# Kernel optimization log

Measured on AMD Instinct MI355X. Metric: run time of the kernel, lower is better.

The kernel has to match this reference:

```python
import jax, jax.numpy as jnp
import numpy as np


def conv1x1(x, w, b):
    # x: [B,C,H,W], w: [O,C], b: [O]
    return jnp.einsum('oc,bchw->bohw', w, x) + b[None, :, None, None]


def interp_bilinear_ac(x, oh, ow):
    # bilinear resize with align_corners=True, x: [B,C,H,W] -> [B,C,oh,ow]
    B, C, H, W = x.shape
    if (H, W) == (oh, ow):
        return x
    ys = jnp.linspace(0.0, H - 1.0, oh)
    xs = jnp.linspace(0.0, W - 1.0, ow)
    y0 = jnp.clip(jnp.floor(ys).astype(jnp.int32), 0, H - 1)
    y1 = jnp.minimum(y0 + 1, H - 1)
    x0 = jnp.clip(jnp.floor(xs).astype(jnp.int32), 0, W - 1)
    x1 = jnp.minimum(x0 + 1, W - 1)
    wy = (ys - y0).astype(x.dtype)
    wx = (xs - x0).astype(x.dtype)
    top = x[:, :, y0, :] * (1 - wy)[None, None, :, None] + x[:, :, y1, :] * wy[None, None, :, None]
    out = top[:, :, :, x0] * (1 - wx)[None, None, None, :] + top[:, :, :, x1] * wx[None, None, None, :]
    return out


def non_local(x, qw, qb, kw, kb, vw, vb, ow_, ob):
    B, C, H, W = x.shape
    HW = H * W
    q = conv1x1(x, qw, qb).reshape(B, -1, HW)  # [B, Ci, HW]
    k = conv1x1(x, kw, kb).reshape(B, -1, HW)
    v = conv1x1(x, vw, vb).reshape(B, -1, HW)
    attn = jnp.einsum('bci,bcj->bij', q, k)     # [B, HW, HW]
    attn = jax.nn.softmax(attn, axis=-1)
    out = jnp.einsum('bcj,bij->bci', v, attn)   # [B, Ci, HW]
    out = out.reshape(B, -1, H, W)
    return conv1x1(out, ow_, ob)


def _forward(x1, x2, x3, x4, qw, qb, kw, kb, vw, vb, ow_, ob, g1w, g1b, g2w, g2b):
    H1, W1 = x1.shape[2], x1.shape[3]
    x2_up = interp_bilinear_ac(x2, H1, W1)
    x3_up = interp_bilinear_ac(x3, H1, W1)
    x4_up = interp_bilinear_ac(x4, H1, W1)
    gf = jnp.concatenate([x1, x2_up, x3_up, x4_up], axis=1)  # [B, 128, H1, W1]
    gf = non_local(gf, qw, qb, kw, kb, vw, vb, ow_, ob)
    h = jax.nn.relu(conv1x1(gf, g1w, g1b))
    sw = jax.nn.sigmoid(conv1x1(h, g2w, g2b))                # [B, 128, H1, W1]
    w1, w2, w3, w4 = sw[:, :32], sw[:, 32:64], sw[:, 64:96], sw[:, 96:128]
    x1_out = x1 * (1 + w1)
    x2_out = x2 * (1 + interp_bilinear_ac(w2, x2.shape[2], x2.shape[3]))
    x3_out = x3 * (1 + interp_bilinear_ac(w3, x3.shape[2], x3.shape[3]))
    x4_out = x4 * (1 + interp_bilinear_ac(w4, x4.shape[2], x4.shape[3]))
    return (x1_out, x2_out, x3_out, x4_out)


def setup_inputs() -> dict:
    key = jax.random.key(0)
    ks = jax.random.split(key, 16)
    C = 128  # channel*4
    Ci = 64  # inter_channel
    Cg = 32
    d = {
        'x1': jax.random.normal(ks[0], (8, 32, 64, 64), jnp.float32),
        'x2': jax.random.normal(ks[1], (8, 32, 32, 32), jnp.float32),
        'x3': jax.random.normal(ks[2], (8, 32, 16, 16), jnp.float32),
        'x4': jax.random.normal(ks[3], (8, 32, 8, 8), jnp.float32),
        'qw': jax.random.normal(ks[4], (Ci, C), jnp.float32) * 0.05,
        'qb': jnp.zeros((Ci,), jnp.float32),
        'kw': jax.random.normal(ks[5], (Ci, C), jnp.float32) * 0.05,
        'kb': jnp.zeros((Ci,), jnp.float32),
        'vw': jax.random.normal(ks[6], (Ci, C), jnp.float32) * 0.05,
        'vb': jnp.zeros((Ci,), jnp.float32),
        'ow_': jax.random.normal(ks[7], (C, Ci), jnp.float32) * 0.05,
        'ob': jnp.zeros((C,), jnp.float32),
        'g1w': jax.random.normal(ks[8], (Cg, C), jnp.float32) * 0.05,
        'g1b': jnp.zeros((Cg,), jnp.float32),
        'g2w': jax.random.normal(ks[9], (C, Cg), jnp.float32) * 0.05,
        'g2b': jnp.zeros((C,), jnp.float32),
    }
    return d


def reference(x1, x2, x3, x4, qw, qb, kw, kb, vw, vb, ow_, ob, g1w, g1b, g2w, g2b):
    return _forward(x1, x2, x3, x4, qw, qb, kw, kb, vw, vb, ow_, ob, g1w, g1b, g2w, g2b)
```

## Files before the change

kernel.cpp:

```cpp
#include <hip/hip_runtime.h>
#include <hip/hip_bf16.h>


typedef __attribute__((ext_vector_type(8))) short s16x8;
typedef __attribute__((ext_vector_type(4))) float f32x4;

#define LOG2E 1.44269504088896340736f

__device__ __forceinline__ unsigned int f2bf(float f) {
    unsigned int u = __float_as_uint(f);
    u += 0x7fffu + ((u >> 16) & 1u);
    return u >> 16;
}
__device__ __forceinline__ unsigned int pk2bf(float a, float b) {
    union { __hip_bfloat162 h; unsigned int u; } cv;
    cv.h = __float22bfloat162_rn(make_float2(a, b));
    return cv.u;
}
__device__ __forceinline__ float bf2f(unsigned short u) {
    return __uint_as_float((unsigned int)u << 16);
}
__device__ __forceinline__ float fexp2(float x) { return __builtin_amdgcn_exp2f(x); }
__device__ __forceinline__ float frcp(float x)  { return __builtin_amdgcn_rcpf(x); }
__device__ __forceinline__ s16x8 cvt8(const float* __restrict__ p, float scale) {
    float4 a = ((const float4*)p)[0];
    float4 b = ((const float4*)p)[1];
    union { s16x8 v; uint4 u; } cv;
    cv.u.x = pk2bf(a.x * scale, a.y * scale);
    cv.u.y = pk2bf(a.z * scale, a.w * scale);
    cv.u.z = pk2bf(b.x * scale, b.y * scale);
    cv.u.w = pk2bf(b.z * scale, b.w * scale);
    return cv.v;
}

__global__ __launch_bounds__(256, 4) void k_qkv(
    const float* __restrict__ x1, const float* __restrict__ x2,
    const float* __restrict__ x3, const float* __restrict__ x4,
    const float* __restrict__ qw, const float* __restrict__ qb,
    const float* __restrict__ kw, const float* __restrict__ kb,
    const float* __restrict__ vw, const float* __restrict__ vb,
    unsigned short* __restrict__ Qg, unsigned short* __restrict__ Kg,
    unsigned short* __restrict__ Vg) {
  __shared__ __align__(16) unsigned short gfb[32 * 136];
  unsigned int* gfbu = (unsigned int*)gfb;

  const int blk = blockIdx.x;
  const int b = blk >> 7;
  const int i0 = (blk & 127) << 5;
  const int t = threadIdx.x;
  const int wv = t >> 6, lane = t & 63;
  const int r = lane & 15, qd = lane >> 4;
  f32x4 zf = {0.f, 0.f, 0.f, 0.f};

  {
    const int cp = t >> 2, q = t & 3;
    const int c0 = cp << 1;
    const int pbase = q << 3;
    const int oy = i0 >> 6;
    const int ox0 = (i0 & 63) | (q << 3);

    if (cp < 16) {
      const float* s0 = x1 + (((b * 32 + c0) << 12) + (oy << 6) + ox0);
      const float* s1 = s0 + 4096;
      #pragma unroll
      for (int k4 = 0; k4 < 2; k4++) {
        float4 va = ((const float4*)s0)[k4];
        float4 vb = ((const float4*)s1)[k4];
        int p = pbase + k4 * 4;
        gfbu[(p + 0) * 68 + cp] = pk2bf(va.x, vb.x);
        gfbu[(p + 1) * 68 + cp] = pk2bf(va.y, vb.y);
        gfbu[(p + 2) * 68 + cp] = pk2bf(va.z, vb.z);
        gfbu[(p + 3) * 68 + cp] = pk2bf(va.w, vb.w);
      }
    } else {
      const float* base; int S, cs;
      if (cp < 32)      { base = x2; S = 32; cs = c0 - 32; }
      else if (cp < 48) { base = x3; S = 16; cs = c0 - 64; }
      else              { base = x4; S = 8;  cs = c0 - 96; }
      const float* pl0 = base + (b * 32 + cs) * S * S;
      const float* pl1 = pl0 + S * S;
      float yf = (float)oy * (float)(S - 1) * (1.0f / 63.0f);
      int y0 = (int)yf; if (y0 > S - 1) y0 = S - 1;
      int y1 = y0 + 1;  if (y1 > S - 1) y1 = S - 1;
      float wy = yf - (float)y0;
      const float* r00 = pl0 + y0 * S; const float* r01 = pl0 + y1 * S;
      const float* r10 = pl1 + y0 * S; const float* r11 = pl1 + y1 * S;
      for (int k = 0; k < 8; k++) {
        int ox = ox0 + k;
        float xf = (float)ox * (float)(S - 1) * (1.0f / 63.0f);
        int xx0 = (int)xf; if (xx0 > S - 1) xx0 = S - 1;
        int xx1 = xx0 + 1; if (xx1 > S - 1) xx1 = S - 1;
        float wx = xf - (float)xx0;
        float a0 = r00[xx0] + wx * (r00[xx1] - r00[xx0]);
        float b0 = r01[xx0] + wx * (r01[xx1] - r01[xx0]);
        float v0 = a0 + wy * (b0 - a0);
        float a1 = r10[xx0] + wx * (r10[xx1] - r10[xx0]);
        float b1 = r11[xx0] + wx * (r11[xx1] - r11[xx0]);
        float v1 = a1 + wy * (b1 - a1);
        gfbu[(pbase + k) * 68 + cp] = pk2bf(v0, v1);
      }
    }
  }
  __syncthreads();

  const int ocb = wv * 48;
  s16x8 af[3][4];
  float4 bias[3];
  #pragma unroll
  for (int mti = 0; mti < 3; mti++) {
    const int goc = ocb + mti * 16;
    const float* wsrc; const float* bsrc; float scale;
    if (goc < 64)       { wsrc = qw + goc * 128;         bsrc = qb + goc;         scale = LOG2E; }
    else if (goc < 128) { wsrc = kw + (goc - 64) * 128;  bsrc = kb + (goc - 64);  scale = 1.0f; }
    else                { wsrc = vw + (goc - 128) * 128; bsrc = vb + (goc - 128); scale = 1.0f; }
    #pragma unroll
    for (int ks = 0; ks < 4; ks++)
      af[mti][ks] = cvt8(wsrc + r * 128 + ks * 32 + qd * 8, scale);
    float4 bv = *(const float4*)(bsrc + qd * 4);
    bias[mti] = make_float4(bv.x * scale, bv.y * scale, bv.z * scale, bv.w * scale);
  }

  #pragma unroll
  for (int nt = 0; nt < 2; nt++) {
    s16x8 bfr[4];
    #pragma unroll
    for (int ks = 0; ks < 4; ks++)
      bfr[ks] = *(const s16x8*)&gfb[(nt * 16 + r) * 136 + ks * 32 + qd * 8];
    f32x4 acc[3] = {zf, zf, zf};
    #pragma unroll
    for (int ks = 0; ks < 4; ks++)
      #pragma unroll
      for (int mti = 0; mti < 3; mti++)
        acc[mti] = __builtin_amdgcn_mfma_f32_16x16x32_bf16(af[mti][ks], bfr[ks], acc[mti], 0, 0, 0);

    const int pos = i0 + nt * 16 + r;
    #pragma unroll
    for (int mti = 0; mti < 3; mti++) {
      const int gmt = wv * 3 + mti;
      float ax = acc[mti].x + bias[mti].x;
      float ay = acc[mti].y + bias[mti].y;
      float az = acc[mti].z + bias[mti].z;
      float aw = acc[mti].w + bias[mti].w;
      if (gmt < 4) {
        uint2 w; w.x = pk2bf(ax, ay); w.y = pk2bf(az, aw);
        *(uint2*)&Qg[(((b << 12) + pos) << 6) + gmt * 16 + qd * 4] = w;
      } else if (gmt < 8) {
        uint2 w; w.x = pk2bf(ax, ay); w.y = pk2bf(az, aw);
        *(uint2*)&Kg[(((b << 12) + pos) << 6) + (gmt - 4) * 16 + qd * 4] = w;
      } else {
        int ocv = (gmt - 8) * 16 + qd * 4;
        Vg[((b * 64 + ocv + 0) << 12) + pos] = (unsigned short)f2bf(ax);
        Vg[((b * 64 + ocv + 1) << 12) + pos] = (unsigned short)f2bf(ay);
        Vg[((b * 64 + ocv + 2) << 12) + pos] = (unsigned short)f2bf(az);
        Vg[((b * 64 + ocv + 3) << 12) + pos] = (unsigned short)f2bf(aw);
      }
    }
  }
}

__global__ __launch_bounds__(256, 4) void k_attn(
    const unsigned short* __restrict__ Qg, const unsigned short* __restrict__ Kg,
    const unsigned short* __restrict__ Vg, unsigned short* __restrict__ Op,
    float* __restrict__ Lp) {
  __shared__ __align__(16) unsigned short Kl[64 * 72];
  __shared__ __align__(16) unsigned short Vl[64 * 72];
  __shared__ __align__(16) unsigned short Pl[4][32 * 72];

  const int b = blockIdx.x >> 7;
  const int part = (blockIdx.x >> 5) & 3;
  const int qg = blockIdx.x & 31;
  const int i0 = qg << 7;
  const int t = threadIdx.x;
  const int wv = t >> 6, lane = t & 63;
  const int r = lane & 15, qd = lane >> 4;
  const int qbase = i0 + wv * 32;

  s16x8 qf[2][2];
  #pragma unroll
  for (int nt = 0; nt < 2; nt++)
    #pragma unroll
    for (int ks = 0; ks < 2; ks++)
      qf[nt][ks] = *(const s16x8*)&Qg[(((b << 12) + qbase + nt * 16 + r) << 6) + ks * 32 + qd * 8];

  f32x4 zf = {0.f, 0.f, 0.f, 0.f};
  f32x4 acc[2][4];
  #pragma unroll
  for (int nt = 0; nt < 2; nt++)
    #pragma unroll
    for (int mt = 0; mt < 4; mt++) acc[nt][mt] = zf;
  f32x4 accl[2] = {zf, zf};

  const short ob = (r == 0) ? (short)0x3F80 : (short)0;
  const s16x8 vones = {ob, ob, ob, ob, ob, ob, ob, ob};

  const int srow = t >> 3, sseg = t & 7;
  const unsigned short* kt0 = &Kg[(((b << 12) + (part << 10) + srow) << 6) + sseg * 8];
  const unsigned short* vt0 = &Vg[((b * 64 + srow) << 12) + (part << 10) + sseg * 8];
  uint4 pk0 = *(const uint4*)(kt0);
  uint4 pk1 = *(const uint4*)(kt0 + (32 << 6));
  uint4 pv0 = *(const uint4*)(vt0);
  uint4 pv1 = *(const uint4*)(vt0 + (32 << 12));

  for (int it = 0; it < 16; it++) {
    __syncthreads();
    *(uint4*)&Kl[srow * 72 + sseg * 8] = pk0;
    *(uint4*)&Kl[(srow + 32) * 72 + sseg * 8] = pk1;
    *(uint4*)&Vl[srow * 72 + sseg * 8] = pv0;
    *(uint4*)&Vl[(srow + 32) * 72 + sseg * 8] = pv1;
    __syncthreads();
    if (it < 15) {
      int j0 = (it + 1) << 6;
      pk0 = *(const uint4*)(kt0 + (j0 << 6));
      pk1 = *(const uint4*)(kt0 + ((j0 + 32) << 6));
      pv0 = *(const uint4*)(vt0 + j0);
      pv1 = *(const uint4*)(vt0 + (32 << 12) + j0);
    }

    #pragma unroll
    for (int mt = 0; mt < 4; mt++) {
      s16x8 kf0 = *(const s16x8*)&Kl[(mt * 16 + r) * 72 + qd * 8];
      s16x8 kf1 = *(const s16x8*)&Kl[(mt * 16 + r) * 72 + 32 + qd * 8];
      #pragma unroll
      for (int nt = 0; nt < 2; nt++) {
        f32x4 s = __builtin_amdgcn_mfma_f32_16x16x32_bf16(kf0, qf[nt][0], zf, 0, 0, 0);
        s = __builtin_amdgcn_mfma_f32_16x16x32_bf16(kf1, qf[nt][1], s, 0, 0, 0);
        float px = fexp2(s.x);
        float py = fexp2(s.y);
        float pz = fexp2(s.z);
        float pw = fexp2(s.w);
        uint2 w;
        w.x = pk2bf(px, py);
        w.y = pk2bf(pz, pw);
        *(uint2*)&Pl[wv][(nt * 16 + r) * 72 + mt * 16 + qd * 4] = w;
      }
    }
    __builtin_amdgcn_wave_barrier();

    #pragma unroll
    for (int ks = 0; ks < 2; ks++) {
      s16x8 pf0 = *(const s16x8*)&Pl[wv][(r) * 72 + ks * 32 + qd * 8];
      s16x8 pf1 = *(const s16x8*)&Pl[wv][(16 + r) * 72 + ks * 32 + qd * 8];
      #pragma unroll
      for (int mt = 0; mt < 4; mt++) {
        s16x8 vf = *(const s16x8*)&Vl[(mt * 16 + r) * 72 + ks * 32 + qd * 8];
        acc[0][mt] = __builtin_amdgcn_mfma_f32_16x16x32_bf16(vf, pf0, acc[0][mt], 0, 0, 0);
        acc[1][mt] = __builtin_amdgcn_mfma_f32_16x16x32_bf16(vf, pf1, acc[1][mt], 0, 0, 0);
      }
      accl[0] = __builtin_amdgcn_mfma_f32_16x16x32_bf16(vones, pf0, accl[0], 0, 0, 0);
      accl[1] = __builtin_amdgcn_mfma_f32_16x16x32_bf16(vones, pf1, accl[1], 0, 0, 0);
    }
  }

  #pragma unroll
  for (int nt = 0; nt < 2; nt++) {
    float lv = __shfl(accl[nt].x, r);
    float inv = frcp(lv);
    int qrow = qbase + nt * 16 + r;
    unsigned short* orow = &Op[(((part * 8 + b) << 12) + qrow) << 6];
    #pragma unroll
    for (int mt = 0; mt < 4; mt++) {
      uint2 w;
      w.x = pk2bf(acc[nt][mt].x * inv, acc[nt][mt].y * inv);
      w.y = pk2bf(acc[nt][mt].z * inv, acc[nt][mt].w * inv);
      *(uint2*)&orow[mt * 16 + qd * 4] = w;
    }
    if (qd == 0) Lp[((part * 8 + b) << 12) + qrow] = lv;
  }
}

__global__ __launch_bounds__(256, 4) void k_out(
    const unsigned short* __restrict__ Op, const float* __restrict__ Lp,
    const float* __restrict__ ow, const float* __restrict__ obias,
    const float* __restrict__ g1w, const float* __restrict__ g1b,
    const float* __restrict__ g2w, const float* __restrict__ g2b,
    const float* __restrict__ x1, float* __restrict__ out,
    unsigned short* __restrict__ SWb) {
  __shared__ __align__(16) unsigned short Ot[32 * 72];
  __shared__ __align__(16) unsigned short gf2t[32 * 136];
  __shared__ __align__(16) unsigned short ht[32 * 40];
  const int blk = blockIdx.x;
  const int b = blk >> 7;
  const int i0 = (blk & 127) << 5;
  const int t = threadIdx.x;
  const int wv = t >> 6, lane = t & 63;
  const int r = lane & 15, qd = lane >> 4;
  f32x4 zf = {0.f, 0.f, 0.f, 0.f};

  {
    const int pos = t >> 3, seg = t & 7;
    const int i = i0 + pos;
    float lp4[4], lsum = 0.f;
    #pragma unroll
    for (int p = 0; p < 4; p++) { lp4[p] = Lp[((p * 8 + b) << 12) + i]; lsum += lp4[p]; }
    float o[8];
    #pragma unroll
    for (int k = 0; k < 8; k++) o[k] = 0.f;
    float invs = frcp(lsum);
    #pragma unroll
    for (int p = 0; p < 4; p++) {
      float w = lp4[p] * invs;
      uint4 u = *(const uint4*)&Op[((((p * 8 + b) << 12) + i) << 6) + seg * 8];
      o[0] += w * __uint_as_float(u.x << 16);
      o[1] += w * __uint_as_float(u.x & 0xFFFF0000u);
      o[2] += w * __uint_as_float(u.y << 16);
      o[3] += w * __uint_as_float(u.y & 0xFFFF0000u);
      o[4] += w * __uint_as_float(u.z << 16);
      o[5] += w * __uint_as_float(u.z & 0xFFFF0000u);
      o[6] += w * __uint_as_float(u.w << 16);
      o[7] += w * __uint_as_float(u.w & 0xFFFF0000u);
    }
    unsigned int* dst = (unsigned int*)&Ot[pos * 72 + seg * 8];
    #pragma unroll
    for (int k = 0; k < 4; k++) dst[k] = pk2bf(o[2 * k], o[2 * k + 1]);
  }
  __syncthreads();

  {
    const int ocb = wv * 32;
    s16x8 af[2][2];
    #pragma unroll
    for (int mt = 0; mt < 2; mt++)
      #pragma unroll
      for (int ks = 0; ks < 2; ks++)
        af[mt][ks] = cvt8(&ow[(ocb + mt * 16 + r) * 64 + ks * 32 + qd * 8], 1.0f);
    float4 bias[2];
    #pragma unroll
    for (int mt = 0; mt < 2; mt++)
      bias[mt] = *(const float4*)&obias[ocb + mt * 16 + qd * 4];
    #pragma unroll
    for (int nt = 0; nt < 2; nt++) {
      s16x8 bfr[2];
      #pragma unroll
      for (int ks = 0; ks < 2; ks++)
        bfr[ks] = *(const s16x8*)&Ot[(nt * 16 + r) * 72 + ks * 32 + qd * 8];
      f32x4 acc[2] = {zf, zf};
      #pragma unroll
      for (int ks = 0; ks < 2; ks++)
        #pragma unroll
        for (int mt = 0; mt < 2; mt++)
          acc[mt] = __builtin_amdgcn_mfma_f32_16x16x32_bf16(af[mt][ks], bfr[ks], acc[mt], 0, 0, 0);
      #pragma unroll
      for (int mt = 0; mt < 2; mt++) {
        uint2 w;
        w.x = pk2bf(acc[mt].x + bias[mt].x, acc[mt].y + bias[mt].y);
        w.y = pk2bf(acc[mt].z + bias[mt].z, acc[mt].w + bias[mt].w);
        *(uint2*)&gf2t[(nt * 16 + r) * 136 + ocb + mt * 16 + qd * 4] = w;
      }
    }
  }
  __syncthreads();

  {
    const int mt = wv & 1, pt = wv >> 1;
    s16x8 af[4];
    #pragma unroll
    for (int ks = 0; ks < 4; ks++)
      af[ks] = cvt8(&g1w[(mt * 16 + r) * 128 + ks * 32 + qd * 8], 1.0f);
    float4 bias = *(const float4*)&g1b[mt * 16 + qd * 4];
    s16x8 bfr[4];
    #pragma unroll
    for (int ks = 0; ks < 4; ks++)
      bfr[ks] = *(const s16x8*)&gf2t[(pt * 16 + r) * 136 + ks * 32 + qd * 8];
    f32x4 acc = zf;
    #pragma unroll
    for (int ks = 0; ks < 4; ks++)
      acc = __builtin_amdgcn_mfma_f32_16x16x32_bf16(af[ks], bfr[ks], acc, 0, 0, 0);
    uint2 w;
    w.x = pk2bf(fmaxf(acc.x + bias.x, 0.f), fmaxf(acc.y + bias.y, 0.f));
    w.y = pk2bf(fmaxf(acc.z + bias.z, 0.f), fmaxf(acc.w + bias.w, 0.f));
    *(uint2*)&ht[(pt * 16 + r) * 40 + mt * 16 + qd * 4] = w;
  }
  __syncthreads();

  {
    const int nb = wv * 32;
    s16x8 bfg[2];
    float bias[2];
    #pragma unroll
    for (int ntl = 0; ntl < 2; ntl++) {
      bfg[ntl] = cvt8(&g2w[(nb + ntl * 16 + r) * 32 + qd * 8], 1.0f);
      bias[ntl] = g2b[nb + ntl * 16 + r];
    }
    #pragma unroll
    for (int mt = 0; mt < 2; mt++) {
      s16x8 af = *(const s16x8*)&ht[(mt * 16 + r) * 40 + qd * 8];
      #pragma unroll
      for (int ntl = 0; ntl < 2; ntl++) {
        f32x4 acc = __builtin_amdgcn_mfma_f32_16x16x32_bf16(af, bfg[ntl], zf, 0, 0, 0);
        const int oc3 = nb + ntl * 16 + r;
        float s0 = frcp(1.0f + fexp2(-LOG2E * (acc.x + bias[ntl])));
        float s1 = frcp(1.0f + fexp2(-LOG2E * (acc.y + bias[ntl])));
        float s2 = frcp(1.0f + fexp2(-LOG2E * (acc.z + bias[ntl])));
        float s3 = frcp(1.0f + fexp2(-LOG2E * (acc.w + bias[ntl])));
        if (nb == 0) {
          const int off = ((b * 32 + oc3) << 12) + i0 + mt * 16 + qd * 4;
          float4 xv = *(const float4*)&x1[off];
          float4 o4;
          o4.x = xv.x * (1.f + s0); o4.y = xv.y * (1.f + s1);
          o4.z = xv.z * (1.f + s2); o4.w = xv.w * (1.f + s3);
          *(float4*)&out[off] = o4;
        } else {
          uint2 w; w.x = pk2bf(s0, s1); w.y = pk2bf(s2, s3);
          *(uint2*)&SWb[((b * 128 + oc3) << 12) + i0 + mt * 16 + qd * 4] = w;
        }
      }
    }
  }
}

__device__ __forceinline__ float bilin64(const unsigned short* __restrict__ p,
                                         int oy, int ox, int n) {
  float yf = (float)oy * 63.0f / (float)n;
  int y0 = (int)yf; if (y0 > 63) y0 = 63;
  int y1 = y0 + 1;  if (y1 > 63) y1 = 63;
  float wy = yf - (float)y0;
  float xf = (float)ox * 63.0f / (float)n;
  int x0 = (int)xf; if (x0 > 63) x0 = 63;
  int x1 = x0 + 1;  if (x1 > 63) x1 = 63;
  float wx = xf - (float)x0;
  float v00 = bf2f(p[y0 * 64 + x0]), v01 = bf2f(p[y0 * 64 + x1]);
  float v10 = bf2f(p[y1 * 64 + x0]), v11 = bf2f(p[y1 * 64 + x1]);
  float top = v00 + wx * (v01 - v00);
  float bot = v10 + wx * (v11 - v10);
  return top + wy * (bot - top);
}

__global__ __launch_bounds__(256) void k_final(
    const float* __restrict__ x2, const float* __restrict__ x3,
    const float* __restrict__ x4,
    const unsigned short* __restrict__ SWb, float* __restrict__ out) {
  const int N1 = 1048576, N2 = 262144, N3 = 65536, N4 = 16384;
  int idx = blockIdx.x * 256 + threadIdx.x;
  if (idx < N2) {
    int b = idx >> 15, rr = idx & 32767;
    int c = rr >> 10, oy = (rr >> 5) & 31, ox = rr & 31;
    float w = bilin64(SWb + ((b * 128 + 32 + c) << 12), oy, ox, 31);
    out[N1 + idx] = x2[idx] * (1.f + w);
  } else if (idx < N2 + N3) {
    int i3 = idx - N2;
    int b = i3 >> 13, rr = i3 & 8191;
    int c = rr >> 8, oy = (rr >> 4) & 15, ox = rr & 15;
    float w = bilin64(SWb + ((b * 128 + 64 + c) << 12), oy, ox, 15);
    out[N1 + idx] = x3[i3] * (1.f + w);
  } else if (idx < N2 + N3 + N4) {
    int i4 = idx - N2 - N3;
    int b = i4 >> 11, rr = i4 & 2047;
    int c = rr >> 6, oy = (rr >> 3) & 7, ox = rr & 7;
    float w = bilin64(SWb + ((b * 128 + 96 + c) << 12), oy, ox, 7);
    out[N1 + idx] = x4[i4] * (1.f + w);
  }
}

extern "C" void kernel_launch(void* const* d_in, const int* in_sizes, int n_in,
                              void* d_out, int out_size, void* d_ws, size_t ws_size,
                              hipStream_t stream) {
  const float* x1  = (const float*)d_in[0];
  const float* x2  = (const float*)d_in[1];
  const float* x3  = (const float*)d_in[2];
  const float* x4  = (const float*)d_in[3];
  const float* qw  = (const float*)d_in[4];
  const float* qb  = (const float*)d_in[5];
  const float* kw  = (const float*)d_in[6];
  const float* kb  = (const float*)d_in[7];
  const float* vw  = (const float*)d_in[8];
  const float* vb  = (const float*)d_in[9];
  const float* ow  = (const float*)d_in[10];
  const float* ob  = (const float*)d_in[11];
  const float* g1w = (const float*)d_in[12];
  const float* g1b = (const float*)d_in[13];
  const float* g2w = (const float*)d_in[14];
  const float* g2b = (const float*)d_in[15];
  float* out = (float*)d_out;

  char* ws = (char*)d_ws;
  unsigned short* Qg  = (unsigned short*)(ws + 0);
  unsigned short* Kg  = (unsigned short*)(ws + 4194304);
  unsigned short* Vg  = (unsigned short*)(ws + 8388608);
  unsigned short* SWb = (unsigned short*)(ws + 0);
  unsigned short* Op  = (unsigned short*)(ws + 12582912);
  float* Lp   = (float*)(ws + 29360128);

  k_qkv<<<1024, 256, 0, stream>>>(x1, x2, x3, x4, qw, qb, kw, kb, vw, vb,
                                  Qg, Kg, Vg);
  k_attn<<<1024, 256, 0, stream>>>(Qg, Kg, Vg, Op, Lp);
  k_out<<<1024, 256, 0, stream>>>(Op, Lp, ow, ob, g1w, g1b, g2w, g2b,
                                  x1, out, SWb);
  k_final<<<1344, 256, 0, stream>>>(x2, x3, x4, SWb, out);
}
```

Before: 179.0 us.

## Use 32x32x16 MFMA in attention and keep P in registers via lane shuffles

The attention kernel moves from 16x16x32 MFMA tiles to 32x32x16 tiles. The softmax probabilities are now repacked between lanes with cross-half shuffles instead of going through a per-wave LDS scratch buffer. The row-sum is accumulated with scalar adds plus one final xor-shuffle, replacing the extra MFMA against a ones vector. This cuts LDS traffic, wave barriers and redundant MFMA work, but relies on a subtle lane-to-element mapping for the P operand and the output store, and the larger accumulators raise register pressure.

After: 183.7 us. 1.03x slower.

```diff
diff --git a/kernel.cpp b/kernel.cpp
--- a/kernel.cpp
+++ b/kernel.cpp
@@ -4,6 +4,7 @@
 
 typedef __attribute__((ext_vector_type(8))) short s16x8;
 typedef __attribute__((ext_vector_type(4))) float f32x4;
+typedef __attribute__((ext_vector_type(16))) float f32x16;
 
 #define LOG2E 1.44269504088896340736f
 
@@ -164,7 +165,6 @@
     float* __restrict__ Lp) {
   __shared__ __align__(16) unsigned short Kl[64 * 72];
   __shared__ __align__(16) unsigned short Vl[64 * 72];
-  __shared__ __align__(16) unsigned short Pl[4][32 * 72];
 
   const int b = blockIdx.x >> 7;
   const int part = (blockIdx.x >> 5) & 3;
@@ -172,26 +172,20 @@
   const int i0 = qg << 7;
   const int t = threadIdx.x;
   const int wv = t >> 6, lane = t & 63;
-  const int r = lane & 15, qd = lane >> 4;
+  const int q = lane & 31, hi = lane >> 5;
   const int qbase = i0 + wv * 32;
 
-  s16x8 qf[2][2];
+  s16x8 qf[4];
   #pragma unroll
-  for (int nt = 0; nt < 2; nt++)
-    #pragma unroll
-    for (int ks = 0; ks < 2; ks++)
-      qf[nt][ks] = *(const s16x8*)&Qg[(((b << 12) + qbase + nt * 16 + r) << 6) + ks * 32 + qd * 8];
-
-  f32x4 zf = {0.f, 0.f, 0.f, 0.f};
-  f32x4 acc[2][4];
+  for (int kc = 0; kc < 4; kc++)
+    qf[kc] = *(const s16x8*)&Qg[(((b << 12) + qbase + q) << 6) + kc * 16 + hi * 8];
+
+  f32x16 acc[2];
   #pragma unroll
-  for (int nt = 0; nt < 2; nt++)
-    #pragma unroll
-    for (int mt = 0; mt < 4; mt++) acc[nt][mt] = zf;
-  f32x4 accl[2] = {zf, zf};
-
-  const short ob = (r == 0) ? (short)0x3F80 : (short)0;
-  const s16x8 vones = {ob, ob, ob, ob, ob, ob, ob, ob};
+  for (int m = 0; m < 2; m++)
+    #pragma unroll
+    for (int e = 0; e < 16; e++) acc[m][e] = 0.f;
+  float ls = 0.f;
 
   const int srow = t >> 3, sseg = t & 7;
   const unsigned short* kt0 = &Kg[(((b << 12) + (part << 10) + srow) << 6) + sseg * 8];
@@ -216,56 +210,67 @@
       pv1 = *(const uint4*)(vt0 + (32 << 12) + j0);
     }
 
-    #pragma unroll
-    for (int mt = 0; mt < 4; mt++) {
-      s16x8 kf0 = *(const s16x8*)&Kl[(mt * 16 + r) * 72 + qd * 8];
-      s16x8 kf1 = *(const s16x8*)&Kl[(mt * 16 + r) * 72 + 32 + qd * 8];
-      #pragma unroll
-      for (int nt = 0; nt < 2; nt++) {
-        f32x4 s = __builtin_amdgcn_mfma_f32_16x16x32_bf16(kf0, qf[nt][0], zf, 0, 0, 0);
-        s = __builtin_amdgcn_mfma_f32_16x16x32_bf16(kf1, qf[nt][1], s, 0, 0, 0);
-        float px = fexp2(s.x);
-        float py = fexp2(s.y);
-        float pz = fexp2(s.z);
-        float pw = fexp2(s.w);
-        uint2 w;
-        w.x = pk2bf(px, py);
-        w.y = pk2bf(pz, pw);
-        *(uint2*)&Pl[wv][(nt * 16 + r) * 72 + mt * 16 + qd * 4] = w;
-      }
-    }
-    __builtin_amdgcn_wave_barrier();
-
-    #pragma unroll
-    for (int ks = 0; ks < 2; ks++) {
-      s16x8 pf0 = *(const s16x8*)&Pl[wv][(r) * 72 + ks * 32 + qd * 8];
-      s16x8 pf1 = *(const s16x8*)&Pl[wv][(16 + r) * 72 + ks * 32 + qd * 8];
-      #pragma unroll
-      for (int mt = 0; mt < 4; mt++) {
-        s16x8 vf = *(const s16x8*)&Vl[(mt * 16 + r) * 72 + ks * 32 + qd * 8];
-        acc[0][mt] = __builtin_amdgcn_mfma_f32_16x16x32_bf16(vf, pf0, acc[0][mt], 0, 0, 0);
-        acc[1][mt] = __builtin_amdgcn_mfma_f32_16x16x32_bf16(vf, pf1, acc[1][mt], 0, 0, 0);
-      }
-      accl[0] = __builtin_amdgcn_mfma_f32_16x16x32_bf16(vones, pf0, accl[0], 0, 0, 0);
-      accl[1] = __builtin_amdgcn_mfma_f32_16x16x32_bf16(vones, pf1, accl[1], 0, 0, 0);
-    }
-  }
-
+    unsigned int pu[2][8];
+    #pragma unroll
+    for (int kt = 0; kt < 2; kt++) {
+      f32x16 st;
+      #pragma unroll
+      for (int e = 0; e < 16; e++) st[e] = 0.f;
+      #pragma unroll
+      for (int kc = 0; kc < 4; kc++) {
+        s16x8 kf = *(const s16x8*)&Kl[(kt * 32 + q) * 72 + kc * 16 + hi * 8];
+        st = __builtin_amdgcn_mfma_f32_32x32x16_bf16(kf, qf[kc], st, 0, 0, 0);
+      }
+      float lsum = 0.f;
+      #pragma unroll
+      for (int i2 = 0; i2 < 8; i2++) {
+        float p0 = fexp2(st[2 * i2]);
+        float p1 = fexp2(st[2 * i2 + 1]);
+        lsum += p0 + p1;
+        pu[kt][i2] = pk2bf(p0, p1);
+      }
+      ls += lsum;
+    }
+
+    #pragma unroll
+    for (int kt = 0; kt < 2; kt++) {
+      #pragma unroll
+      for (int c16 = 0; c16 < 2; c16++) {
+        const int c16g = kt * 2 + c16;
+        unsigned int a0 = pu[kt][c16 * 4 + 0], a1 = pu[kt][c16 * 4 + 1];
+        unsigned int a2 = pu[kt][c16 * 4 + 2], a3 = pu[kt][c16 * 4 + 3];
+        unsigned int k0 = hi ? a2 : a0, k1 = hi ? a3 : a1;
+        unsigned int s0 = hi ? a0 : a2, s1 = hi ? a1 : a3;
+        unsigned int r0 = __shfl_xor(s0, 32);
+        unsigned int r1 = __shfl_xor(s1, 32);
+        union { s16x8 v; unsigned int u[4]; } pb;
+        pb.u[0] = hi ? r0 : k0;
+        pb.u[1] = hi ? r1 : k1;
+        pb.u[2] = hi ? k0 : r0;
+        pb.u[3] = hi ? k1 : r1;
+        #pragma unroll
+        for (int mtv = 0; mtv < 2; mtv++) {
+          s16x8 vf = *(const s16x8*)&Vl[(mtv * 32 + q) * 72 + c16g * 16 + hi * 8];
+          acc[mtv] = __builtin_amdgcn_mfma_f32_32x32x16_bf16(vf, pb.v, acc[mtv], 0, 0, 0);
+        }
+      }
+    }
+  }
+
+  ls += __shfl_xor(ls, 32);
+  float inv = frcp(ls);
+  const int qrow = qbase + q;
+  unsigned short* orow = &Op[(((part * 8 + b) << 12) + qrow) << 6];
   #pragma unroll
-  for (int nt = 0; nt < 2; nt++) {
-    float lv = __shfl(accl[nt].x, r);
-    float inv = frcp(lv);
-    int qrow = qbase + nt * 16 + r;
-    unsigned short* orow = &Op[(((part * 8 + b) << 12) + qrow) << 6];
-    #pragma unroll
-    for (int mt = 0; mt < 4; mt++) {
-      uint2 w;
-      w.x = pk2bf(acc[nt][mt].x * inv, acc[nt][mt].y * inv);
-      w.y = pk2bf(acc[nt][mt].z * inv, acc[nt][mt].w * inv);
-      *(uint2*)&orow[mt * 16 + qd * 4] = w;
-    }
-    if (qd == 0) Lp[((part * 8 + b) << 12) + qrow] = lv;
-  }
+  for (int mtv = 0; mtv < 2; mtv++) {
+    #pragma unroll
+    for (int i2 = 0; i2 < 8; i2++) {
+      int dbase = ((2 * i2) & 3) + 8 * ((2 * i2) >> 2) + 4 * hi + mtv * 32;
+      *(unsigned int*)&orow[dbase] =
+          pk2bf(acc[mtv][2 * i2] * inv, acc[mtv][2 * i2 + 1] * inv);
+    }
+  }
+  if (hi == 0) Lp[((part * 8 + b) << 12) + qrow] = ls;
 }
 
 __global__ __launch_bounds__(256, 4) void k_out(
```
